# Optimization experiments

Hardware: AMD Instinct MI355X
Metric: run time of the kernel (lower is better)

The kernel has to match this reference:

```python
import jax, jax.numpy as jnp
import numpy as np

B, S, N, D, M = 4, 4096, 16, 64, 4  # batch, seq, heads, head_dim, num_scales

def setup_inputs() -> dict:
    key = jax.random.key(0)
    ks = jax.random.split(key, 6)
    return {
        "q": jax.random.normal(ks[0], (B, S, N, D), dtype=jnp.float32),
        "k": jax.random.normal(ks[1], (B, S, N, D), dtype=jnp.float32),
        "v": jax.random.normal(ks[2], (B, S, N, D), dtype=jnp.float32),
        "memory": jax.random.normal(ks[3], (B, M, N, D, D), dtype=jnp.float32),
        "decay_factors": jax.random.uniform(ks[4], (M,), dtype=jnp.float32) + 0.5,
        "gate_weights": jax.random.uniform(ks[5], (M,), dtype=jnp.float32),
    }

def reference(q, k, v, memory, decay_factors, gate_weights):
    # --- update_memory: decayed outer-product accumulation ---
    # new_info[b,n,k,v] = sum_s k[b,s,n,k] * v[b,s,n,v]  (fused; never build [b,s,n,k,v])
    new_info = jnp.einsum('bsnk,bsnv->bnkv', k, v)
    sig = jax.nn.sigmoid(decay_factors)            # [M]
    sig5 = sig[None, :, None, None, None]          # [1,M,1,1,1]
    mem_new = memory * sig5 + (1.0 - sig5) * new_info[:, None]  # [B,M,N,D,D]
    # --- forward read: q @ memory per scale, softmax-gated scale mixing ---
    gates = jax.nn.softmax(gate_weights)           # [M]
    # fuse gate mixing into the contraction; never build [b,m,s,n,v]
    out = jnp.einsum('bsnk,bmnkv,m->bsnv', q, mem_new, gates)
    return out
```

## Files before the change

kernel.cpp:

```cpp
#include <hip/hip_runtime.h>
#include <hip/hip_bf16.h>
#include <math.h>

constexpr int B = 4, S = 4096, N = 16, D = 64, M = 4;
constexpr int SND = S * N * D;
constexpr int ND  = N * D;
constexpr int DD  = D * D;
constexpr int NCH = 8;
constexpr int SPB = S / NCH;
constexpr int NST = 16;

typedef __attribute__((ext_vector_type(8))) short bf16x8;
typedef __attribute__((ext_vector_type(4))) float f32x4;
typedef unsigned short u16;
typedef unsigned int u32;

__device__ inline u16 f2bf(float x) {
  __hip_bfloat16 h = __float2bfloat16(x);
  return __builtin_bit_cast(u16, h);
}

__device__ inline void gload16(const float* g, float* l) {
  __builtin_amdgcn_global_load_lds(
      (const __attribute__((address_space(1))) void*)g,
      (__attribute__((address_space(3))) void*)l, 16, 0, 0);
}

__global__ __launch_bounds__(256) void k1_partials(const float* __restrict__ kg,
                                                   const float* __restrict__ vg,
                                                   u16* __restrict__ part) {
  __shared__ float kbuf[4][32][64];
  __shared__ float vbuf[4][32][64];

  const int t = threadIdx.x, w = t >> 6, l = t & 63;
  const int lr = l & 15, lg = l >> 4;
  const int bn = blockIdx.x, ch = blockIdx.y;
  const int b = bn >> 4, n = bn & 15;
  const size_t base = (size_t)b * SND + (size_t)n * D;
  const int s0 = ch * SPB;

  f32x4 acc[4];
#pragma unroll
  for (int i = 0; i < 4; ++i) acc[i] = (f32x4)0.f;

#define STAGE(st, bi)                                                        \
  {                                                                          \
    _Pragma("unroll") for (int i = 0; i < 2; ++i) {                          \
      const int gid = (w * 2 + i) * 64 + l;              \
      const int sl = gid >> 4;                                \
      const int cg = (gid & 15) ^ ((sl >> 3) & 3); \
      const float* gk = kg + base + (size_t)(s0 + (st) * 32 + sl) * ND + cg * 4; \
      const float* gv = vg + base + (size_t)(s0 + (st) * 32 + sl) * ND + cg * 4; \
      gload16(gk, &kbuf[bi][0][0] + (w * 2 + i) * 256);                      \
      gload16(gv, &vbuf[bi][0][0] + (w * 2 + i) * 256);                      \
    }                                                                        \
  }

#define COMPUTE(bi)                                                          \
  {                                                                          \
    bf16x8 af, bq[4];                                                        \
    _Pragma("unroll") for (int j = 0; j < 8; ++j)                            \
      af[j] = (short)f2bf(                                                   \
          kbuf[bi][8 * lg + j][(((4 * w + (lr >> 2)) ^ lg) << 2) + (lr & 3)]); \
    _Pragma("unroll") for (int ni = 0; ni < 4; ++ni)                         \
    _Pragma("unroll") for (int j = 0; j < 8; ++j)                            \
      bq[ni][j] = (short)f2bf(                                               \
          vbuf[bi][8 * lg + j][(((4 * ni + (lr >> 2)) ^ lg) << 2) + (lr & 3)]); \
    _Pragma("unroll") for (int ni = 0; ni < 4; ++ni)                         \
      acc[ni] = __builtin_amdgcn_mfma_f32_16x16x32_bf16(af, bq[ni],          \
                                                        acc[ni], 0, 0, 0);   \
  }

#define WAITBAR(n)                                                           \
  asm volatile("s_waitcnt vmcnt(" #n ")" ::: "memory");                      \
  __builtin_amdgcn_s_barrier();                                              \
  __builtin_amdgcn_sched_barrier(0);

  STAGE(0, 0);
  STAGE(1, 1);
  STAGE(2, 2);
  WAITBAR(8);

#pragma unroll
  for (int st = 0; st < NST; ++st) {
    if (st + 3 < NST) STAGE(st + 3, (st + 3) & 3);
    COMPUTE(st & 3);
    if (st < NST - 3)       { WAITBAR(8); }
    else if (st == NST - 3) { WAITBAR(4); }
    else if (st == NST - 2) { WAITBAR(0); }
  }

#undef STAGE
#undef COMPUTE
#undef WAITBAR

  u16* p = part + ((size_t)bn * NCH + ch) * DD;
#pragma unroll
  for (int ni = 0; ni < 4; ++ni)
#pragma unroll
    for (int ri = 0; ri < 4; ++ri)
      p[(16 * w + 4 * lg + ri) * 64 + 16 * ni + lr] = f2bf(acc[ni][ri]);
}

__global__ __launch_bounds__(256) void k2_combine(const u16* __restrict__ part,
                                                  const float* __restrict__ memg,
                                                  const float* __restrict__ decay,
                                                  const float* __restrict__ gatew,
                                                  u16* __restrict__ meffT) {
  const int t = threadIdx.x;
  const int bn = blockIdx.x;
  const int b = bn >> 4, n = bn & 15;
  const int kv = blockIdx.y * 256 + t;
  const int k = kv >> 6, v = kv & 63;

  float gw[M], df[M];
#pragma unroll
  for (int m = 0; m < M; ++m) { gw[m] = gatew[m]; df[m] = decay[m]; }
  const float mx = fmaxf(fmaxf(gw[0], gw[1]), fmaxf(gw[2], gw[3]));
  float e[M], esum = 0.f;
#pragma unroll
  for (int m = 0; m < M; ++m) { e[m] = expf(gw[m] - mx); esum += e[m]; }
  float wgt[M], cc = 0.f;
#pragma unroll
  for (int m = 0; m < M; ++m) {
    const float g = e[m] / esum;
    const float sg = 1.f / (1.f + expf(-df[m]));
    wgt[m] = g * sg;
    cc += g * (1.f - sg);
  }

  const u16* pb = part + (size_t)bn * NCH * DD + kv;
  float ni = 0.f;
#pragma unroll
  for (int ch = 0; ch < NCH; ++ch) {
    __hip_bfloat16 h = __builtin_bit_cast(__hip_bfloat16, pb[(size_t)ch * DD]);
    ni += __bfloat162float(h);
  }
  float a = cc * ni;
#pragma unroll
  for (int m = 0; m < M; ++m)
    a += wgt[m] * memg[(((size_t)b * M + m) * N + n) * DD + kv];

  meffT[(size_t)bn * DD + v * 64 + k] = f2bf(a);
}

__global__ __launch_bounds__(256, 4) void k3_out(const float* __restrict__ qg,
                                                 const u16* __restrict__ meffT,
                                                 float* __restrict__ outg) {
  const int t = threadIdx.x, w = t >> 6, l = t & 63;
  const int lr = l & 15, lg = l >> 4;
  const int bn = blockIdx.x;
  const int b = bn >> 4, n = bn & 15;
  const int s0 = blockIdx.y * 256 + w * 64;

  const u16* mb = meffT + (size_t)bn * DD;
  bf16x8 bfr[4][2];
#pragma unroll
  for (int ni = 0; ni < 4; ++ni)
#pragma unroll
    for (int ks = 0; ks < 2; ++ks)
      bfr[ni][ks] = *(const bf16x8*)(mb + (16 * ni + lr) * 64 + 32 * ks + 8 * lg);

  f32x4 acc[4][4];
#pragma unroll
  for (int i = 0; i < 4; ++i)
#pragma unroll
    for (int j = 0; j < 4; ++j) acc[i][j] = (f32x4)0.f;

  const size_t qbase = (size_t)b * SND + (size_t)n * D;

#pragma unroll
  for (int mi = 0; mi < 4; ++mi) {
    const float* qr = qg + qbase + (size_t)(s0 + 16 * mi + lr) * ND + 8 * lg;
#pragma unroll
    for (int ks = 0; ks < 2; ++ks) {
      float qa[8];
      *(float4*)&qa[0] = *(const float4*)(qr + 32 * ks);
      *(float4*)&qa[4] = *(const float4*)(qr + 32 * ks + 4);
      bf16x8 a;
#pragma unroll
      for (int j = 0; j < 8; ++j) a[j] = (short)f2bf(qa[j]);
#pragma unroll
      for (int ni = 0; ni < 4; ++ni)
        acc[mi][ni] = __builtin_amdgcn_mfma_f32_16x16x32_bf16(a, bfr[ni][ks],
                                                              acc[mi][ni], 0, 0, 0);
    }
  }

#pragma unroll
  for (int mi = 0; mi < 4; ++mi)
#pragma unroll
    for (int ni = 0; ni < 4; ++ni)
#pragma unroll
      for (int ri = 0; ri < 4; ++ri)
        outg[qbase + (size_t)(s0 + 16 * mi + 4 * lg + ri) * ND + 16 * ni + lr] =
            acc[mi][ni][ri];
}

extern "C" void kernel_launch(void* const* d_in, const int* in_sizes, int n_in,
                              void* d_out, int out_size, void* d_ws, size_t ws_size,
                              hipStream_t stream) {
  const float* q     = (const float*)d_in[0];
  const float* k     = (const float*)d_in[1];
  const float* v     = (const float*)d_in[2];
  const float* memg  = (const float*)d_in[3];
  const float* decay = (const float*)d_in[4];
  const float* gatew = (const float*)d_in[5];
  float* out = (float*)d_out;

  u16* meffT = (u16*)d_ws;
  const size_t meffT_bytes = (size_t)64 * DD * sizeof(u16);
  u16* part = (u16*)((char*)d_ws + meffT_bytes);

  hipLaunchKernelGGL(k1_partials, dim3(64, NCH), dim3(256), 0, stream,
                     k, v, part);
  hipLaunchKernelGGL(k2_combine, dim3(64, 16), dim3(256), 0, stream,
                     part, memg, decay, gatew, meffT);
  hipLaunchKernelGGL(k3_out, dim3(64, 16), dim3(256), 0, stream,
                     q, meffT, out);
}
```

Measured before the change: 61.15 us.

## Deepen k1 load pipeline with smaller 16-row stages and unswizzled LDS layout

Splits the k/v staging in the partial outer-product kernel into 16-row stages across 8 LDS buffers, with up to seven stages in flight instead of three. Each MFMA step now reads two adjacent 16-row buffers as one 32-row K slice, so compute runs on every other iteration. The XOR column swizzle is removed for a plain row-major layout. The aim is more memory-level parallelism to hide global load latency, at the cost of more barriers and likely LDS bank conflicts on the strided reads.

Result: no change. 60.28 us (-1.4%).

```diff
diff --git a/kernel.cpp b/kernel.cpp
--- a/kernel.cpp
+++ b/kernel.cpp
@@ -8,7 +8,7 @@
 constexpr int DD  = D * D;
 constexpr int NCH = 8;
 constexpr int SPB = S / NCH;
-constexpr int NST = 16;
+constexpr int NST = 32;
 
 typedef __attribute__((ext_vector_type(8))) short bf16x8;
 typedef __attribute__((ext_vector_type(4))) float f32x4;
@@ -29,8 +29,8 @@
 __global__ __launch_bounds__(256) void k1_partials(const float* __restrict__ kg,
                                                    const float* __restrict__ vg,
                                                    u16* __restrict__ part) {
-  __shared__ float kbuf[4][32][64];
-  __shared__ float vbuf[4][32][64];
+  __shared__ float kbuf[8][16][64];
+  __shared__ float vbuf[8][16][64];
 
   const int t = threadIdx.x, w = t >> 6, l = t & 63;
   const int lr = l & 15, lg = l >> 4;
@@ -45,49 +45,48 @@
 
 #define STAGE(st, bi)                                                        \
   {                                                                          \
-    _Pragma("unroll") for (int i = 0; i < 2; ++i) {                          \
-      const int gid = (w * 2 + i) * 64 + l;              \
-      const int sl = gid >> 4;                                \
-      const int cg = (gid & 15) ^ ((sl >> 3) & 3); \
-      const float* gk = kg + base + (size_t)(s0 + (st) * 32 + sl) * ND + cg * 4; \
-      const float* gv = vg + base + (size_t)(s0 + (st) * 32 + sl) * ND + cg * 4; \
-      gload16(gk, &kbuf[bi][0][0] + (w * 2 + i) * 256);                      \
-      gload16(gv, &vbuf[bi][0][0] + (w * 2 + i) * 256);                      \
-    }                                                                        \
-  }
-
-#define COMPUTE(bi)                                                          \
+    const int sl = 4 * w + (l >> 4), cf = (l & 15) * 4;                      \
+    const float* gk = kg + base + (size_t)(s0 + (st) * 16 + sl) * ND + cf;   \
+    const float* gv = vg + base + (size_t)(s0 + (st) * 16 + sl) * ND + cf;   \
+    gload16(gk, &kbuf[bi][0][0] + w * 256);                                  \
+    gload16(gv, &vbuf[bi][0][0] + w * 256);                                  \
+  }
+
+#define COMPUTE(biA)                                                         \
   {                                                                          \
+    const float* kb = &kbuf[biA][0][0];                                      \
+    const float* vb = &vbuf[biA][0][0];                                      \
+    const int lo = (lg >> 1) * 1024 + (8 * (lg & 1)) * 64;                   \
     bf16x8 af, bq[4];                                                        \
     _Pragma("unroll") for (int j = 0; j < 8; ++j)                            \
-      af[j] = (short)f2bf(                                                   \
-          kbuf[bi][8 * lg + j][(((4 * w + (lr >> 2)) ^ lg) << 2) + (lr & 3)]); \
+      af[j] = (short)f2bf(kb[lo + j * 64 + 16 * w + lr]);                    \
     _Pragma("unroll") for (int ni = 0; ni < 4; ++ni)                         \
     _Pragma("unroll") for (int j = 0; j < 8; ++j)                            \
-      bq[ni][j] = (short)f2bf(                                               \
-          vbuf[bi][8 * lg + j][(((4 * ni + (lr >> 2)) ^ lg) << 2) + (lr & 3)]); \
+      bq[ni][j] = (short)f2bf(vb[lo + j * 64 + 16 * ni + lr]);               \
     _Pragma("unroll") for (int ni = 0; ni < 4; ++ni)                         \
       acc[ni] = __builtin_amdgcn_mfma_f32_16x16x32_bf16(af, bq[ni],          \
                                                         acc[ni], 0, 0, 0);   \
   }
 
-#define WAITBAR(n)                                                           \
-  asm volatile("s_waitcnt vmcnt(" #n ")" ::: "memory");                      \
+#define WAITBAR(nlit)                                                        \
+  asm volatile("s_waitcnt vmcnt(" #nlit ")" ::: "memory");                   \
   __builtin_amdgcn_s_barrier();                                              \
   __builtin_amdgcn_sched_barrier(0);
 
-  STAGE(0, 0);
-  STAGE(1, 1);
-  STAGE(2, 2);
-  WAITBAR(8);
+  STAGE(0, 0); STAGE(1, 1); STAGE(2, 2); STAGE(3, 3);
+  STAGE(4, 4); STAGE(5, 5); STAGE(6, 6);
+  WAITBAR(12);
 
 #pragma unroll
   for (int st = 0; st < NST; ++st) {
-    if (st + 3 < NST) STAGE(st + 3, (st + 3) & 3);
-    COMPUTE(st & 3);
-    if (st < NST - 3)       { WAITBAR(8); }
-    else if (st == NST - 3) { WAITBAR(4); }
-    else if (st == NST - 2) { WAITBAR(0); }
+    if (st & 1) COMPUTE((st - 1) & 7);
+    if      (st <= 25) { WAITBAR(10); }
+    else if (st == 26) { WAITBAR(8); }
+    else if (st == 27) { WAITBAR(6); }
+    else if (st == 28) { WAITBAR(4); }
+    else if (st == 29) { WAITBAR(2); }
+    else if (st == 30) { WAITBAR(0); }
+    if (st + 7 < NST) STAGE(st + 7, (st + 7) & 7);
   }
 
 #undef STAGE
```
